# Optimization experiments

Measured on AMD Instinct MI355X. Metric: run time of the kernel, lower is better.

## Reference

```python
import jax, jax.numpy as jnp
import numpy as np

D_MODEL = 2048
N_HEADS = 16
HEAD_DIM = 128
WINDOW = 512
ROPE_BASE = 10000.0
B, N = 2, 2048
INNER = N_HEADS * HEAD_DIM


def setup_inputs() -> dict:
    key = jax.random.key(0)
    k1, k2, k3 = jax.random.split(key, 3)
    x = jax.random.normal(k1, (B, N, D_MODEL), dtype=jnp.float32)
    # torch nn.Linear stores weight as [out_features, in_features]
    w_qkv = jax.random.normal(k2, (3 * INNER, D_MODEL), dtype=jnp.float32) / np.sqrt(D_MODEL)
    w_o = jax.random.normal(k3, (D_MODEL, INNER), dtype=jnp.float32) / np.sqrt(INNER)
    return {"x": x, "w_qkv": w_qkv, "w_o": w_o}


def _rotate_half(t):
    t1, t2 = jnp.split(t, 2, axis=-1)
    return jnp.concatenate([-t2, t1], axis=-1)


def _rope(q, k, offset=0):
    # q, k: [B, H, N, D]; GPT-NeoX half-split rotary embedding
    D = q.shape[-1]
    inv_freq = 1.0 / (ROPE_BASE ** (jnp.arange(0, D, 2, dtype=jnp.float32) / D))
    pos = jnp.arange(q.shape[2], dtype=jnp.float32) + offset
    ang = pos[:, None] * inv_freq[None, :]                 # [N, D/2]
    cos = jnp.concatenate([jnp.cos(ang), jnp.cos(ang)], axis=-1)  # [N, D]
    sin = jnp.concatenate([jnp.sin(ang), jnp.sin(ang)], axis=-1)
    q_r = q * cos + _rotate_half(q) * sin
    k_r = k * cos + _rotate_half(k) * sin
    return q_r, k_r


def reference(x, w_qkv, w_o):
    Bq, Nq, _ = x.shape
    # QKV projection (no bias)
    qkv = jnp.einsum('bnd,ed->bne', x, w_qkv)              # [B, N, 3*INNER]
    q, k, v = jnp.split(qkv, 3, axis=-1)
    def to_heads(t):
        return t.reshape(Bq, Nq, N_HEADS, HEAD_DIM).transpose(0, 2, 1, 3)  # [B,H,N,D]
    q, k, v = to_heads(q), to_heads(k), to_heads(v)
    q, k = _rope(q, k, offset=0)
    # sliding-window causal mask: valid key j for query i iff (i - WINDOW) < j <= i
    i = jnp.arange(Nq)[:, None]
    j = jnp.arange(Nq)[None, :]
    valid = (j > i - WINDOW) & (j <= i)                    # [N, N]
    scale = 1.0 / np.sqrt(HEAD_DIM)
    scores = jnp.einsum('bhnd,bhkd->bhnk', q, k) * scale   # [B,H,N,N]
    scores = jnp.where(valid[None, None], scores, -jnp.inf)
    att = jax.nn.softmax(scores, axis=-1)
    out = jnp.einsum('bhnk,bhkd->bhnd', att, v)
    out = out.transpose(0, 2, 1, 3).reshape(Bq, Nq, INNER)
    y = jnp.einsum('bni,di->bnd', out, w_o)
    return y
```

## Files before the change

kernel.cpp:

```cpp
#include <hip/hip_runtime.h>
#include <hip/hip_bf16.h>
#include <cstdint>

typedef __bf16 bf16x8 __attribute__((ext_vector_type(8)));
typedef float floatx4 __attribute__((ext_vector_type(4)));

__device__ __forceinline__ void gl2lds16(const void* g, void* l) {
  __builtin_amdgcn_global_load_lds(
      (const __attribute__((address_space(1))) unsigned int*)g,
      (__attribute__((address_space(3))) unsigned int*)(uintptr_t)l,
      16, 0, 0);
}

__global__ __launch_bounds__(256)
void cvt_kernel(const float* __restrict__ in, __hip_bfloat16* __restrict__ out, int n) {
  int i = (blockIdx.x * 256 + threadIdx.x) * 4;
  if (i >= n) return;
  const float4 v = *(const float4*)(in + i);
  out[i + 0] = __float2bfloat16(v.x);
  out[i + 1] = __float2bfloat16(v.y);
  out[i + 2] = __float2bfloat16(v.z);
  out[i + 3] = __float2bfloat16(v.w);
}

__global__ __launch_bounds__(256)
void gemm_bt(const __hip_bfloat16* __restrict__ A, const __hip_bfloat16* __restrict__ Bm,
             void* __restrict__ Cp, int M, int Nc, int K, int c_fp32)
{
  __shared__ __hip_bfloat16 As[128 * 32];
  __shared__ __hip_bfloat16 Bs[128 * 32];
  const int tid = threadIdx.x;
  const int lane = tid & 63, wave = tid >> 6;
  const int wm = (wave & 1) * 64, wn = (wave >> 1) * 64;
  const int m0 = blockIdx.x * 128, n0 = blockIdx.y * 128;
  const int lrow = lane & 15, lk = (lane >> 4) * 8;
  floatx4 acc[4][4] = {};
  const int c0 = tid, c1 = tid + 256;
  const int r0 = c0 >> 2, o0 = (c0 & 3) * 8;
  const int r1 = c1 >> 2, o1 = (c1 & 3) * 8;
  for (int kt = 0; kt < K; kt += 32) {
    __syncthreads();
    gl2lds16(A + (size_t)(m0 + r0) * K + kt + o0, &As[c0 * 8]);
    gl2lds16(A + (size_t)(m0 + r1) * K + kt + o1, &As[c1 * 8]);
    gl2lds16(Bm + (size_t)(n0 + r0) * K + kt + o0, &Bs[c0 * 8]);
    gl2lds16(Bm + (size_t)(n0 + r1) * K + kt + o1, &Bs[c1 * 8]);
    __syncthreads();
    bf16x8 af[4], bfr[4];
#pragma unroll
    for (int t = 0; t < 4; t++) af[t] = *(const bf16x8*)&As[(wm + t * 16 + lrow) * 32 + lk];
#pragma unroll
    for (int t = 0; t < 4; t++) bfr[t] = *(const bf16x8*)&Bs[(wn + t * 16 + lrow) * 32 + lk];
#pragma unroll
    for (int mt = 0; mt < 4; mt++)
#pragma unroll
      for (int nt = 0; nt < 4; nt++)
        acc[mt][nt] = __builtin_amdgcn_mfma_f32_16x16x32_bf16(af[mt], bfr[nt], acc[mt][nt], 0, 0, 0);
  }
  const int lq4 = (lane >> 4) * 4;
#pragma unroll
  for (int mt = 0; mt < 4; mt++)
#pragma unroll
    for (int nt = 0; nt < 4; nt++)
#pragma unroll
      for (int r = 0; r < 4; r++) {
        const int m = m0 + wm + mt * 16 + lq4 + r;
        const int n = n0 + wn + nt * 16 + lrow;
        const float v = acc[mt][nt][r];
        if (c_fp32) ((float*)Cp)[(size_t)m * Nc + n] = v;
        else ((__hip_bfloat16*)Cp)[(size_t)m * Nc + n] = __float2bfloat16(v);
      }
}

__global__ __launch_bounds__(512, 2)
void gemm_qkv256(const __hip_bfloat16* __restrict__ A,
                 const __hip_bfloat16* __restrict__ W,
                 __hip_bfloat16* __restrict__ Qr,
                 __hip_bfloat16* __restrict__ Kr,
                 __hip_bfloat16* __restrict__ Vt)
{
  extern __shared__ __hip_bfloat16 sm[];
  const int tid = threadIdx.x, lane = tid & 63, wave = tid >> 6;
  const int wr = wave >> 2, wc = wave & 3;
  const int m0 = blockIdx.x << 8, n0 = blockIdx.y << 8;
  const int lrow = lane & 15, dg = lane >> 4, lq4 = dg * 4;
  const int rslot = (dg ^ ((lrow >> 1) & 3)) * 8;

  const int arow = tid >> 2;
  const int ascol = ((tid & 3) ^ ((tid >> 3) & 3)) * 8;
  const __hip_bfloat16* aS0 = A + (size_t)(m0 + arow) * 2048 + ascol;
  const __hip_bfloat16* aS1 = A + (size_t)(m0 + 128 + arow) * 2048 + ascol;
  const __hip_bfloat16* bS0 = W + (size_t)(n0 + arow) * 2048 + ascol;
  const __hip_bfloat16* bS1 = W + (size_t)(n0 + 128 + arow) * 2048 + ascol;

  floatx4 acc[8][4] = {};

#define STAGE(TT) do {                                        \
    const int bb_ = (TT) & 3; const int kk_ = (TT) * 32;      \
    gl2lds16(aS0 + kk_, &sm[bb_ * 16384 + tid * 8]);          \
    gl2lds16(aS1 + kk_, &sm[bb_ * 16384 + 4096 + tid * 8]);   \
    gl2lds16(bS0 + kk_, &sm[bb_ * 16384 + 8192 + tid * 8]);   \
    gl2lds16(bS1 + kk_, &sm[bb_ * 16384 + 12288 + tid * 8]);  \
  } while (0)

  STAGE(0); STAGE(1); STAGE(2);

#define KSTEP(TT, WIMM, DOSTAGE) do {                                          \
    asm volatile("" ::: "memory");                                             \
    __builtin_amdgcn_s_waitcnt(WIMM);     \
    __builtin_amdgcn_s_barrier();       \
    asm volatile("" ::: "memory");                                             \
    const int bb = (TT) & 3;                                                   \
    if (DOSTAGE) STAGE((TT) + 3);                                              \
    bf16x8 af[8], bfr[4];                                                      \
    _Pragma("unroll")                                                          \
    for (int mt = 0; mt < 8; mt++)                                             \
      af[mt] = *(const bf16x8*)&sm[bb * 16384 + (wr * 128 + mt * 16 + lrow) * 32 + rslot]; \
    _Pragma("unroll")                                                          \
    for (int nt = 0; nt < 4; nt++)                                             \
      bfr[nt] = *(const bf16x8*)&sm[bb * 16384 + 8192 + (wc * 64 + nt * 16 + lrow) * 32 + rslot]; \
    __builtin_amdgcn_s_setprio(1);                                             \
    _Pragma("unroll")                                                          \
    for (int mt = 0; mt < 8; mt++)                                             \
      _Pragma("unroll")                                                        \
      for (int nt = 0; nt < 4; nt++)                                           \
        acc[mt][nt] = __builtin_amdgcn_mfma_f32_16x16x32_bf16(af[mt], bfr[nt], acc[mt][nt], 0, 0, 0); \
    __builtin_amdgcn_s_setprio(0);                                             \
  } while (0)

  for (int t = 0; t < 61; ++t) KSTEP(t, 0x78, true);
  KSTEP(61, 0x78, false);
  KSTEP(62, 0x74, false);
  KSTEP(63, 0x70, false);
#undef KSTEP
#undef STAGE

  const int seg = n0 >> 11;
  const int h0 = (n0 & 2047) >> 7;
  const int b = m0 >> 11;
  const int seq0 = m0 & 2047;
  float* invfp = (float*)((char*)sm + 122880);

  __syncthreads();
  if (seg < 2 && tid < 64) invfp[tid] = __expf(-(float)tid * 0.14391156831212787f);

  const float qs = (seg == 0) ? 0.08838834764831845f : 1.0f;
  for (int p = 0; p < 2; ++p) {
    if (p) __syncthreads();
    if (wr == p) {
      if (seg < 2) {
#pragma unroll
        for (int mt = 0; mt < 8; mt++)
#pragma unroll
          for (int nt = 0; nt < 4; nt++)
#pragma unroll
            for (int r = 0; r < 4; r++)
              sm[(mt * 16 + lq4 + r) * 264 + wc * 64 + nt * 16 + lrow] =
                  __float2bfloat16(acc[mt][nt][r]);
      } else {
#pragma unroll
        for (int mt = 0; mt < 8; mt++)
#pragma unroll
          for (int nt = 0; nt < 4; nt++)
#pragma unroll
            for (int r = 0; r < 4; r++)
              sm[(wc * 64 + nt * 16 + lrow) * 136 + mt * 16 + lq4 + r] =
                  __float2bfloat16(acc[mt][nt][r]);
      }
    }
    __syncthreads();
    if (seg < 2) {
      __hip_bfloat16* Out = seg ? Kr : Qr;
#pragma unroll
      for (int it = 0; it < 4; ++it) {
        const int task = tid + it * 512;
        const int row = task >> 4;
        const int hh = (task >> 3) & 1;
        const int g8 = (task & 7) * 8;
        const int seq = seq0 + p * 128 + row;
        const float pos = (float)seq;
        const bf16x8 lo8 = *(const bf16x8*)&sm[row * 264 + hh * 128 + g8];
        const bf16x8 hi8 = *(const bf16x8*)&sm[row * 264 + hh * 128 + g8 + 64];
        alignas(16) __hip_bfloat16 lo[8], hi[8];
#pragma unroll
        for (int k = 0; k < 8; k++) {
          float sn, cs;
          __sincosf(pos * invfp[g8 + k], &sn, &cs);
          const float a = (float)lo8[k];
          const float bb2 = (float)hi8[k];
          lo[k] = __float2bfloat16((a * cs - bb2 * sn) * qs);
          hi[k] = __float2bfloat16((bb2 * cs + a * sn) * qs);
        }
        const size_t ob = ((size_t)((b * 16 + h0 + hh) * 2048 + seq)) * 128;
        *(bf16x8*)&Out[ob + g8] = *(const bf16x8*)lo;
        *(bf16x8*)&Out[ob + g8 + 64] = *(const bf16x8*)hi;
      }
    } else {
#pragma unroll
      for (int it = 0; it < 8; ++it) {
        const int task = tid + it * 512;
        const int col = task >> 4;
        const int sg = (task & 15) * 8;
        const bf16x8 v8 = *(const bf16x8*)&sm[col * 136 + sg];
        const int hh = col >> 7, d = col & 127;
        *(bf16x8*)&Vt[((size_t)((b * 16 + h0 + hh) * 128 + d)) * 2048 + seq0 + p * 128 + sg] = v8;
      }
    }
  }
}

#define KSTR 136
#define VSTR 72
__global__ __launch_bounds__(512, 4)
void attn_swa(const __hip_bfloat16* __restrict__ Qr, const __hip_bfloat16* __restrict__ Kr,
              const __hip_bfloat16* __restrict__ Vt, __hip_bfloat16* __restrict__ Out)
{
  __shared__ __hip_bfloat16 Ks[64 * KSTR];
  __shared__ __hip_bfloat16 Vs[128 * VSTR];
  __shared__ __hip_bfloat16 Pb[8][16 * VSTR];
  const int qt = blockIdx.x, bh = blockIdx.y;
  const int tid = threadIdx.x, lane = tid & 63, wave = tid >> 6;
  const int lrow = lane & 15, lk = (lane >> 4) * 8, lq4 = (lane >> 4) * 4;
  const int i0 = qt * 128;
  const float NEG_INF = -__builtin_inff();
  const __hip_bfloat16* Qh = Qr + (size_t)bh * 2048 * 128;
  const __hip_bfloat16* Kh = Kr + (size_t)bh * 2048 * 128;
  const __hip_bfloat16* Vh = Vt + (size_t)bh * 128 * 2048;

  const int ck0 = tid, ck1 = tid + 512;
  const int kr0 = ck0 >> 4, kg0 = (ck0 & 15) * 8;
  const int kr1 = ck1 >> 4, kg1 = (ck1 & 15) * 8;
  const int cv0 = tid, cv1 = tid + 512;
  const int vd0 = cv0 >> 3, vc0 = (cv0 & 7) * 8;
  const int vd1 = cv1 >> 3, vc1 = (cv1 & 7) * 8;

  const int iw = i0 + wave * 16 + lrow;
  bf16x8 qf[4];
#pragma unroll
  for (int ks = 0; ks < 4; ks++)
    qf[ks] = *(const bf16x8*)&Qh[(size_t)iw * 128 + ks * 32 + lk];

  floatx4 accO[8] = {};
  float m_i = NEG_INF, l_i = 0.f;
  const int imin = i0 + wave * 16;
  const int lo = i0 - 511;
  const int jt_lo = (lo > 0 ? lo : 0) >> 6;
  const int jt_hi = (i0 + 127) >> 6;

  int j0n = jt_lo * 64;
  int4 rk0 = *(const int4*)&Kh[(size_t)(j0n + kr0) * 128 + kg0];
  int4 rk1 = *(const int4*)&Kh[(size_t)(j0n + kr1) * 128 + kg1];
  int4 rv0 = *(const int4*)&Vh[(size_t)vd0 * 2048 + j0n + vc0];
  int4 rv1 = *(const int4*)&Vh[(size_t)vd1 * 2048 + j0n + vc1];

  for (int jt = jt_lo; jt <= jt_hi; jt++) {
    const int j0 = jt * 64;
    __syncthreads();
    *(int4*)&Ks[kr0 * KSTR + kg0] = rk0;
    *(int4*)&Ks[kr1 * KSTR + kg1] = rk1;
    *(int4*)&Vs[vd0 * VSTR + vc0] = rv0;
    *(int4*)&Vs[vd1 * VSTR + vc1] = rv1;
    if (jt < jt_hi) {
      const int jn = j0 + 64;
      rk0 = *(const int4*)&Kh[(size_t)(jn + kr0) * 128 + kg0];
      rk1 = *(const int4*)&Kh[(size_t)(jn + kr1) * 128 + kg1];
      rv0 = *(const int4*)&Vh[(size_t)vd0 * 2048 + jn + vc0];
      rv1 = *(const int4*)&Vh[(size_t)vd1 * 2048 + jn + vc1];
    }
    asm volatile("" ::: "memory");
    __builtin_amdgcn_s_waitcnt(0xC07F);
    __builtin_amdgcn_s_barrier();
    asm volatile("" ::: "memory");

    floatx4 s[4] = {};
#pragma unroll
    for (int nt = 0; nt < 4; nt++) {
      const int krow = (nt * 16 + lrow) * KSTR;
#pragma unroll
      for (int ks = 0; ks < 4; ks++) {
        const bf16x8 kf = *(const bf16x8*)&Ks[krow + ks * 32 + lk];
        s[nt] = __builtin_amdgcn_mfma_f32_16x16x32_bf16(kf, qf[ks], s[nt], 0, 0, 0);
      }
    }
    const bool full = (j0 + 63 <= imin) && (j0 >= imin + 15 - 511);
    float rmax = NEG_INF;
    if (full) {
#pragma unroll
      for (int nt = 0; nt < 4; nt++)
#pragma unroll
        for (int r = 0; r < 4; r++) rmax = fmaxf(rmax, s[nt][r]);
    } else {
#pragma unroll
      for (int nt = 0; nt < 4; nt++) {
#pragma unroll
        for (int r = 0; r < 4; r++) {
          const int j = j0 + nt * 16 + lq4 + r;
          const float sv = ((j <= iw) && (j > iw - 512)) ? s[nt][r] : NEG_INF;
          s[nt][r] = sv;
          rmax = fmaxf(rmax, sv);
        }
      }
    }
    rmax = fmaxf(rmax, __shfl_xor(rmax, 16));
    rmax = fmaxf(rmax, __shfl_xor(rmax, 32));
    const float mnew = fmaxf(m_i, rmax);
    const float alpha = __expf(fminf(m_i - mnew, 0.f));
    m_i = mnew;
    float rs = 0.f;
    if (full) {
#pragma unroll
      for (int nt = 0; nt < 4; nt++)
#pragma unroll
        for (int r = 0; r < 4; r++) {
          const float p = __expf(s[nt][r] - mnew);
          s[nt][r] = p;
          rs += p;
        }
    } else {
#pragma unroll
      for (int nt = 0; nt < 4; nt++)
#pragma unroll
        for (int r = 0; r < 4; r++) {
          const float sv = s[nt][r];
          const float p = (sv == NEG_INF) ? 0.f : __expf(sv - mnew);
          s[nt][r] = p;
          rs += p;
        }
    }
    rs += __shfl_xor(rs, 16);
    rs += __shfl_xor(rs, 32);
    l_i = l_i * alpha + rs;
#pragma unroll
    for (int dt = 0; dt < 8; dt++) accO[dt] *= alpha;
#pragma unroll
    for (int nt = 0; nt < 4; nt++) {
      alignas(8) __hip_bfloat16 p4[4];
#pragma unroll
      for (int r = 0; r < 4; r++) p4[r] = __float2bfloat16(s[nt][r]);
      *(uint64_t*)&Pb[wave][lrow * VSTR + nt * 16 + lq4] = *(const uint64_t*)p4;
    }
    bf16x8 pf[2];
#pragma unroll
    for (int jf = 0; jf < 2; jf++)
      pf[jf] = *(const bf16x8*)&Pb[wave][lrow * VSTR + jf * 32 + lk];
#pragma unroll
    for (int dt = 0; dt < 8; dt++) {
      const int vrow = (dt * 16 + lrow) * VSTR;
#pragma unroll
      for (int jf = 0; jf < 2; jf++) {
        const bf16x8 vf = *(const bf16x8*)&Vs[vrow + jf * 32 + lk];
        accO[dt] = __builtin_amdgcn_mfma_f32_16x16x32_bf16(vf, pf[jf], accO[dt], 0, 0, 0);
      }
    }
  }
  const int b = bh >> 4, h = bh & 15;
  const float inv_l = 1.0f / l_i;
  const size_t rowb = ((size_t)(b * 2048 + iw)) * 2048 + h * 128;
#pragma unroll
  for (int dt = 0; dt < 8; dt++) {
    alignas(8) __hip_bfloat16 o4[4];
#pragma unroll
    for (int r = 0; r < 4; r++) o4[r] = __float2bfloat16(accO[dt][r] * inv_l);
    *(uint64_t*)&Out[rowb + dt * 16 + lq4] = *(const uint64_t*)o4;
  }
}

extern "C" void kernel_launch(void* const* d_in, const int* in_sizes, int n_in,
                              void* d_out, int out_size, void* d_ws, size_t ws_size,
                              hipStream_t stream)
{
  const float* x = (const float*)d_in[0];
  const float* w_qkv = (const float*)d_in[1];
  const float* w_o = (const float*)d_in[2];
  float* y = (float*)d_out;
  char* ws = (char*)d_ws;

  const size_t SZ_X = 16777216;
  const size_t SZ_WQKV = 25165824;
  const size_t SZ_Q = 16777216;

  __hip_bfloat16* xb = (__hip_bfloat16*)(ws);
  __hip_bfloat16* wqkvb = (__hip_bfloat16*)(ws + SZ_X);
  __hip_bfloat16* Qr = (__hip_bfloat16*)(ws + SZ_X + SZ_WQKV);
  __hip_bfloat16* Kr = (__hip_bfloat16*)(ws + SZ_X + SZ_WQKV + SZ_Q);
  __hip_bfloat16* Vt = (__hip_bfloat16*)(ws + SZ_X + SZ_WQKV + 2 * SZ_Q);

  static bool s_attr_done = false;
  if (!s_attr_done) {
    hipFuncSetAttribute((const void*)gemm_qkv256,
                        hipFuncAttributeMaxDynamicSharedMemorySize, 131072);
    s_attr_done = true;
  }

  cvt_kernel<<<dim3(8192), dim3(256), 0, stream>>>(x, xb, 8388608);
  cvt_kernel<<<dim3(12288), dim3(256), 0, stream>>>(w_qkv, wqkvb, 12582912);
  gemm_qkv256<<<dim3(16, 24), dim3(512), 131072, stream>>>(xb, wqkvb, Qr, Kr, Vt);
  attn_swa<<<dim3(16, 32), dim3(512), 0, stream>>>(Qr, Kr, Vt, xb );
  cvt_kernel<<<dim3(4096), dim3(256), 0, stream>>>(w_o, wqkvb, 4194304);
  gemm_bt<<<dim3(32, 16), dim3(256), 0, stream>>>(xb, wqkvb, (void*)y, 4096, 2048, 2048, 1);
}
```

Before: 363.5 us.

## Use pipelined 256x256 GEMM for output projection and split k-step staging

Replaces the simple single-buffered 128x128 output-projection GEMM with a 256x256-tile kernel that shares the four-stage global-to-LDS pipeline used by the QKV GEMM. The shared k-step is reworked into two half-steps that load A and B fragments separately and issue the next stage's A and B loads between extra barriers, to overlap staging with MFMA work. The output GEMM now launches only 128 blocks, which may underfill the device, and the extra barriers add sync cost to the QKV GEMM.

```diff
diff --git a/kernel.cpp b/kernel.cpp
--- a/kernel.cpp
+++ b/kernel.cpp
@@ -23,53 +23,76 @@
   out[i + 3] = __float2bfloat16(v.w);
 }
 
-__global__ __launch_bounds__(256)
-void gemm_bt(const __hip_bfloat16* __restrict__ A, const __hip_bfloat16* __restrict__ Bm,
-             void* __restrict__ Cp, int M, int Nc, int K, int c_fp32)
-{
-  __shared__ __hip_bfloat16 As[128 * 32];
-  __shared__ __hip_bfloat16 Bs[128 * 32];
-  const int tid = threadIdx.x;
-  const int lane = tid & 63, wave = tid >> 6;
-  const int wm = (wave & 1) * 64, wn = (wave >> 1) * 64;
-  const int m0 = blockIdx.x * 128, n0 = blockIdx.y * 128;
-  const int lrow = lane & 15, lk = (lane >> 4) * 8;
-  floatx4 acc[4][4] = {};
-  const int c0 = tid, c1 = tid + 256;
-  const int r0 = c0 >> 2, o0 = (c0 & 3) * 8;
-  const int r1 = c1 >> 2, o1 = (c1 & 3) * 8;
-  for (int kt = 0; kt < K; kt += 32) {
-    __syncthreads();
-    gl2lds16(A + (size_t)(m0 + r0) * K + kt + o0, &As[c0 * 8]);
-    gl2lds16(A + (size_t)(m0 + r1) * K + kt + o1, &As[c1 * 8]);
-    gl2lds16(Bm + (size_t)(n0 + r0) * K + kt + o0, &Bs[c0 * 8]);
-    gl2lds16(Bm + (size_t)(n0 + r1) * K + kt + o1, &Bs[c1 * 8]);
-    __syncthreads();
-    bf16x8 af[4], bfr[4];
-#pragma unroll
-    for (int t = 0; t < 4; t++) af[t] = *(const bf16x8*)&As[(wm + t * 16 + lrow) * 32 + lk];
-#pragma unroll
-    for (int t = 0; t < 4; t++) bfr[t] = *(const bf16x8*)&Bs[(wn + t * 16 + lrow) * 32 + lk];
-#pragma unroll
-    for (int mt = 0; mt < 4; mt++)
-#pragma unroll
-      for (int nt = 0; nt < 4; nt++)
-        acc[mt][nt] = __builtin_amdgcn_mfma_f32_16x16x32_bf16(af[mt], bfr[nt], acc[mt][nt], 0, 0, 0);
-  }
-  const int lq4 = (lane >> 4) * 4;
-#pragma unroll
-  for (int mt = 0; mt < 4; mt++)
-#pragma unroll
-    for (int nt = 0; nt < 4; nt++)
-#pragma unroll
-      for (int r = 0; r < 4; r++) {
-        const int m = m0 + wm + mt * 16 + lq4 + r;
-        const int n = n0 + wn + nt * 16 + lrow;
-        const float v = acc[mt][nt][r];
-        if (c_fp32) ((float*)Cp)[(size_t)m * Nc + n] = v;
-        else ((__hip_bfloat16*)Cp)[(size_t)m * Nc + n] = __float2bfloat16(v);
-      }
-}
+
+#define GEMM_PREAMBLE(APTR, BPTR)                                              \
+  const int tid = threadIdx.x, lane = tid & 63, wave = tid >> 6;               \
+  const int wr = wave >> 2, wc = wave & 3;                                     \
+  const int m0 = blockIdx.x << 8, n0 = blockIdx.y << 8;                        \
+  const int lrow = lane & 15, dg = lane >> 4, lq4 = dg * 4;                    \
+  const int rslot = (dg ^ ((lrow >> 1) & 3)) * 8;                              \
+  const int arow = tid >> 2;                                                   \
+  const int ascol = ((tid & 3) ^ ((tid >> 3) & 3)) * 8;                        \
+  const __hip_bfloat16* aS0 = (APTR) + (size_t)(m0 + arow) * 2048 + ascol;     \
+  const __hip_bfloat16* aS1 = (APTR) + (size_t)(m0 + 128 + arow) * 2048 + ascol; \
+  const __hip_bfloat16* bS0 = (BPTR) + (size_t)(n0 + arow) * 2048 + ascol;     \
+  const __hip_bfloat16* bS1 = (BPTR) + (size_t)(n0 + 128 + arow) * 2048 + ascol; \
+  floatx4 acc[8][4] = {};
+
+#define STAGE_A(TT) do { const int bb_ = (TT) & 3; const int kk_ = (TT) * 32;  \
+    gl2lds16(aS0 + kk_, &sm[bb_ * 16384 + tid * 8]);                           \
+    gl2lds16(aS1 + kk_, &sm[bb_ * 16384 + 4096 + tid * 8]); } while (0)
+#define STAGE_B(TT) do { const int bb_ = (TT) & 3; const int kk_ = (TT) * 32;  \
+    gl2lds16(bS0 + kk_, &sm[bb_ * 16384 + 8192 + tid * 8]);                    \
+    gl2lds16(bS1 + kk_, &sm[bb_ * 16384 + 12288 + tid * 8]); } while (0)
+
+#define STAGE_AB(TT) do { STAGE_A(TT); STAGE_B(TT); } while (0)
+
+#define MEMFENCE asm volatile("" ::: "memory")
+
+#define KSTEP(TT, WIMM, DOSTAGE) do {                                          \
+    const int bb = (TT) & 3;                                                   \
+    MEMFENCE; __builtin_amdgcn_s_waitcnt(WIMM); MEMFENCE;                      \
+    __builtin_amdgcn_s_barrier();            \
+    MEMFENCE;                                                                  \
+    bf16x8 af0[4], af1[4], bfr[4];                                             \
+    _Pragma("unroll")                                                          \
+    for (int mt = 0; mt < 4; mt++)                                             \
+      af0[mt] = *(const bf16x8*)&sm[bb * 16384 + (wr * 128 + mt * 16 + lrow) * 32 + rslot]; \
+    _Pragma("unroll")                                                          \
+    for (int nt = 0; nt < 4; nt++)                                             \
+      bfr[nt] = *(const bf16x8*)&sm[bb * 16384 + 8192 + (wc * 64 + nt * 16 + lrow) * 32 + rslot]; \
+    if (DOSTAGE) STAGE_A((TT) + 3);                                            \
+    MEMFENCE; __builtin_amdgcn_s_barrier(); MEMFENCE;                          \
+    __builtin_amdgcn_s_waitcnt(0xC07F); MEMFENCE;                              \
+    __builtin_amdgcn_s_setprio(1);                                             \
+    _Pragma("unroll")                                                          \
+    for (int mt = 0; mt < 4; mt++)                                             \
+      _Pragma("unroll")                                                        \
+      for (int nt = 0; nt < 4; nt++)                                           \
+        acc[mt][nt] = __builtin_amdgcn_mfma_f32_16x16x32_bf16(af0[mt], bfr[nt], acc[mt][nt], 0, 0, 0); \
+    __builtin_amdgcn_s_setprio(0);                                             \
+    MEMFENCE; __builtin_amdgcn_s_barrier(); MEMFENCE;                          \
+    _Pragma("unroll")                                                          \
+    for (int mt = 0; mt < 4; mt++)                                             \
+      af1[mt] = *(const bf16x8*)&sm[bb * 16384 + (wr * 128 + 64 + mt * 16 + lrow) * 32 + rslot]; \
+    if (DOSTAGE) STAGE_B((TT) + 3);                                            \
+    MEMFENCE; __builtin_amdgcn_s_barrier(); MEMFENCE;                          \
+    __builtin_amdgcn_s_waitcnt(0xC07F); MEMFENCE;                              \
+    __builtin_amdgcn_s_setprio(1);                                             \
+    _Pragma("unroll")                                                          \
+    for (int mt = 0; mt < 4; mt++)                                             \
+      _Pragma("unroll")                                                        \
+      for (int nt = 0; nt < 4; nt++)                                           \
+        acc[4 + mt][nt] = __builtin_amdgcn_mfma_f32_16x16x32_bf16(af1[mt], bfr[nt], acc[4 + mt][nt], 0, 0, 0); \
+    __builtin_amdgcn_s_setprio(0);                                             \
+  } while (0)
+
+#define GEMM_KLOOP()                                                           \
+  STAGE_AB(0); STAGE_AB(1); STAGE_AB(2);                                       \
+  for (int t = 0; t < 61; ++t) KSTEP(t, 0x0078, true);                         \
+  KSTEP(61, 0x0078, false);                                                    \
+  KSTEP(62, 0x0074, false);                                                    \
+  KSTEP(63, 0x0070, false);
 
 __global__ __launch_bounds__(512, 2)
 void gemm_qkv256(const __hip_bfloat16* __restrict__ A,
@@ -79,60 +102,8 @@
                  __hip_bfloat16* __restrict__ Vt)
 {
   extern __shared__ __hip_bfloat16 sm[];
-  const int tid = threadIdx.x, lane = tid & 63, wave = tid >> 6;
-  const int wr = wave >> 2, wc = wave & 3;
-  const int m0 = blockIdx.x << 8, n0 = blockIdx.y << 8;
-  const int lrow = lane & 15, dg = lane >> 4, lq4 = dg * 4;
-  const int rslot = (dg ^ ((lrow >> 1) & 3)) * 8;
-
-  const int arow = tid >> 2;
-  const int ascol = ((tid & 3) ^ ((tid >> 3) & 3)) * 8;
-  const __hip_bfloat16* aS0 = A + (size_t)(m0 + arow) * 2048 + ascol;
-  const __hip_bfloat16* aS1 = A + (size_t)(m0 + 128 + arow) * 2048 + ascol;
-  const __hip_bfloat16* bS0 = W + (size_t)(n0 + arow) * 2048 + ascol;
-  const __hip_bfloat16* bS1 = W + (size_t)(n0 + 128 + arow) * 2048 + ascol;
-
-  floatx4 acc[8][4] = {};
-
-#define STAGE(TT) do {                                        \
-    const int bb_ = (TT) & 3; const int kk_ = (TT) * 32;      \
-    gl2lds16(aS0 + kk_, &sm[bb_ * 16384 + tid * 8]);          \
-    gl2lds16(aS1 + kk_, &sm[bb_ * 16384 + 4096 + tid * 8]);   \
-    gl2lds16(bS0 + kk_, &sm[bb_ * 16384 + 8192 + tid * 8]);   \
-    gl2lds16(bS1 + kk_, &sm[bb_ * 16384 + 12288 + tid * 8]);  \
-  } while (0)
-
-  STAGE(0); STAGE(1); STAGE(2);
-
-#define KSTEP(TT, WIMM, DOSTAGE) do {                                          \
-    asm volatile("" ::: "memory");                                             \
-    __builtin_amdgcn_s_waitcnt(WIMM);     \
-    __builtin_amdgcn_s_barrier();       \
-    asm volatile("" ::: "memory");                                             \
-    const int bb = (TT) & 3;                                                   \
-    if (DOSTAGE) STAGE((TT) + 3);                                              \
-    bf16x8 af[8], bfr[4];                                                      \
-    _Pragma("unroll")                                                          \
-    for (int mt = 0; mt < 8; mt++)                                             \
-      af[mt] = *(const bf16x8*)&sm[bb * 16384 + (wr * 128 + mt * 16 + lrow) * 32 + rslot]; \
-    _Pragma("unroll")                                                          \
-    for (int nt = 0; nt < 4; nt++)                                             \
-      bfr[nt] = *(const bf16x8*)&sm[bb * 16384 + 8192 + (wc * 64 + nt * 16 + lrow) * 32 + rslot]; \
-    __builtin_amdgcn_s_setprio(1);                                             \
-    _Pragma("unroll")                                                          \
-    for (int mt = 0; mt < 8; mt++)                                             \
-      _Pragma("unroll")                                                        \
-      for (int nt = 0; nt < 4; nt++)                                           \
-        acc[mt][nt] = __builtin_amdgcn_mfma_f32_16x16x32_bf16(af[mt], bfr[nt], acc[mt][nt], 0, 0, 0); \
-    __builtin_amdgcn_s_setprio(0);                                             \
-  } while (0)
-
-  for (int t = 0; t < 61; ++t) KSTEP(t, 0x78, true);
-  KSTEP(61, 0x78, false);
-  KSTEP(62, 0x74, false);
-  KSTEP(63, 0x70, false);
-#undef KSTEP
-#undef STAGE
+  GEMM_PREAMBLE(A, W)
+  GEMM_KLOOP()
 
   const int seg = n0 >> 11;
   const int h0 = (n0 & 2047) >> 7;
@@ -207,6 +178,31 @@
     }
   }
 }
+
+__global__ __launch_bounds__(512, 2)
+void gemm_o256(const __hip_bfloat16* __restrict__ A,
+               const __hip_bfloat16* __restrict__ Wo,
+               float* __restrict__ C)
+{
+  extern __shared__ __hip_bfloat16 sm[];
+  GEMM_PREAMBLE(A, Wo)
+  GEMM_KLOOP()
+#pragma unroll
+  for (int mt = 0; mt < 8; mt++)
+#pragma unroll
+    for (int nt = 0; nt < 4; nt++)
+#pragma unroll
+      for (int r = 0; r < 4; r++)
+        C[(size_t)(m0 + wr * 128 + mt * 16 + lq4 + r) * 2048 +
+          (n0 + wc * 64 + nt * 16 + lrow)] = acc[mt][nt][r];
+}
+
+#undef KSTEP
+#undef GEMM_KLOOP
+#undef STAGE_A
+#undef STAGE_B
+#undef STAGE_AB
+#undef GEMM_PREAMBLE
 
 #define KSTR 136
 #define VSTR 72
@@ -388,6 +384,8 @@
   if (!s_attr_done) {
     hipFuncSetAttribute((const void*)gemm_qkv256,
                         hipFuncAttributeMaxDynamicSharedMemorySize, 131072);
+    hipFuncSetAttribute((const void*)gemm_o256,
+                        hipFuncAttributeMaxDynamicSharedMemorySize, 131072);
     s_attr_done = true;
   }
 
@@ -396,5 +394,5 @@
   gemm_qkv256<<<dim3(16, 24), dim3(512), 131072, stream>>>(xb, wqkvb, Qr, Kr, Vt);
   attn_swa<<<dim3(16, 32), dim3(512), 0, stream>>>(Qr, Kr, Vt, xb );
   cvt_kernel<<<dim3(4096), dim3(256), 0, stream>>>(w_o, wqkvb, 4194304);
-  gemm_bt<<<dim3(32, 16), dim3(256), 0, stream>>>(xb, wqkvb, (void*)y, 4096, 2048, 2048, 1);
-}
+  gemm_o256<<<dim3(16, 8), dim3(512), 131072, stream>>>(xb, wqkvb, y);
+}
```

Result: no change. 361.2 us (-0.6%).
